# Kernel optimization log

Hardware: AMD Instinct MI355X
Metric: run time of the kernel (lower is better)

Reference implementation:

```python
import jax, jax.numpy as jnp
import numpy as np

FEAT = 1433
HID = 2
NUM_CLASS = 7
EPS = 1e-5  # torch BatchNorm1d default eps


def _bn_softsign(h, gamma, beta):
    # BatchNorm1d in training mode: batch stats over (batch, length) per channel.
    mu = h.mean(axis=(0, 2), keepdims=True)
    var = h.var(axis=(0, 2), keepdims=True)  # biased, matches torch normalization
    hn = (h - mu) * jax.lax.rsqrt(var + EPS)
    hn = hn * gamma[None, :, None] + beta[None, :, None]
    return hn / (1.0 + jnp.abs(hn))  # Softsign


def feature_adjacency(x, y):
    # (x.unsqueeze(-1) * y.unsqueeze(-2)).sum(dim=1) with x channel dim == 1
    # reduces to an outer product of x[:,0] with neighbor.sum over K.
    adj = jnp.einsum('bf,bg->bfg', x.sum(1), y.sum(1))  # [B,F,F]
    adj = adj + jnp.swapaxes(adj, -1, -2)
    adj = jnp.sqrt(adj)
    # row_normalize: divide by sum over dim 1, zero out inf/nan
    norm = adj / adj.sum(axis=1, keepdims=True)
    norm = jnp.where(jnp.isfinite(norm), norm, 0.0)
    return norm + jnp.eye(FEAT, dtype=x.dtype)


def featbrd(x, adj, W, b):
    # adjacency-based feature conv: y[b,c,f] = sum_g adj[(b),f,g] x[b,c,g],
    # then 1x1 conv over channels (Conv1d kernel_size=1).
    if adj.shape[0] == 1:
        y = jnp.einsum('fg,bcg->bcf', adj[0], x)
    else:
        y = jnp.einsum('bfg,bcg->bcf', adj, x)
    return jnp.einsum('oc,bcf->bof', W, y) + b[None, :, None]


def setup_inputs() -> dict:
    key = jax.random.key(0)
    ks = jax.random.split(key, 10)
    B, K = 64, 8
    inp = {
        'x': jax.random.uniform(ks[0], (B, 1, FEAT), dtype=jnp.float32),
        'neighbor': jax.random.uniform(ks[1], (B, K, FEAT), dtype=jnp.float32),
        'adj_buf': jnp.zeros((1, FEAT, FEAT), jnp.float32),
        'W1': jax.random.normal(ks[2], (HID, 1), jnp.float32) * 0.5,
        'b1': jnp.zeros((HID,), jnp.float32),
        'W2': jax.random.normal(ks[3], (HID, HID), jnp.float32) * 0.5,
        'b2': jnp.zeros((HID,), jnp.float32),
        'g1': jnp.ones((HID,), jnp.float32),
        'be1': jnp.zeros((HID,), jnp.float32),
        'g2': jnp.ones((HID,), jnp.float32),
        'be2': jnp.zeros((HID,), jnp.float32),
        'Wc': jax.random.normal(ks[4], (NUM_CLASS, FEAT * HID), jnp.float32) * 0.02,
        'bc': jnp.zeros((NUM_CLASS,), jnp.float32),
    }
    return inp


def reference(x, neighbor, adj_buf, W1, b1, W2, b2, g1, be1, g2, be2, Wc, bc):
    fadj = feature_adjacency(x, neighbor)          # [B,F,F]
    adj_tot = adj_buf + fadj.sum(0)                # [1,F,F] (buffer starts at zero)
    h = _bn_softsign(featbrd(x, fadj, W1, b1), g1, be1)      # [B,HID,F]
    h = _bn_softsign(featbrd(h, adj_tot, W2, b2), g2, be2)   # [B,HID,F]
    flat = h.reshape(h.shape[0], -1)               # Flatten (C then F, row-major)
    return flat @ Wc.T + bc
```

## Files before the change

kernel.cpp:

```cpp
#include <hip/hip_runtime.h>
#include <hip/hip_bf16.h>
#include <math.h>

constexpr int F   = 1433;
constexpr int NB  = 64;
constexpr int KN  = 8;
constexpr int BF  = NB * F;
constexpr float EPS = 1e-5f;

constexpr int SF  = 16;
constexpr int CH  = (F + SF - 1) / SF;
constexpr int SK  = 8;
constexpr int KCH = (F + SK - 1) / SK;
constexpr int FT  = 16;

constexpr int O_YS  = 0;
constexpr int O_Q   = O_YS + BF;
constexpr int O_DP  = O_Q + BF;
constexpr int O_Y1P = O_DP + SF * BF;
constexpr int O_Y1  = O_Y1P + SF * BF;
constexpr int O_HT  = O_Y1 + BF;
constexpr int O_Y2  = O_HT + 128 * F;
constexpr int O_AB  = O_Y2 + 2 * BF;
constexpr int O_ST  = O_AB + 1026752;

__global__ __launch_bounds__(256) void k_D(const float* __restrict__ x,
                                           const float* __restrict__ nbr,
                                           float* __restrict__ DP,
                                           float* __restrict__ ys_out) {
  __shared__ __align__(16) float2 xy[F];
  const int b = blockIdx.x, s = blockIdx.y;
  for (int i = threadIdx.x; i < F; i += 256) {
    const float* p = nbr + (size_t)b * KN * F + i;
    float acc = 0.f;
#pragma unroll
    for (int k = 0; k < KN; ++k) acc += p[k * F];
    xy[i] = make_float2(x[b * F + i], acc);
  }
  __syncthreads();
  if (s == 0) {
    for (int i = threadIdx.x; i < F; i += 256) ys_out[b * F + i] = xy[i].y;
  }
  const int cs = s * CH, cn = min(CH, F - cs);
  float gx[6], gy[6], acc[6] = {};
#pragma unroll
  for (int j = 0; j < 6; ++j) {
    int g = threadIdx.x + 256 * j;
    float2 p = (g < F) ? xy[g] : make_float2(0.f, 0.f);
    gx[j] = p.x; gy[j] = p.y;
  }
  for (int i = 0; i < cn; ++i) {
    float2 p = xy[cs + i];
#pragma unroll
    for (int j = 0; j < 6; ++j)
      acc[j] += __builtin_amdgcn_sqrtf(fmaf(gy[j], p.x, gx[j] * p.y));
  }
#pragma unroll
  for (int j = 0; j < 6; ++j) {
    int g = threadIdx.x + 256 * j;
    if (g < F) DP[(size_t)s * BF + b * F + g] = acc[j];
  }
}

__global__ __launch_bounds__(256) void k_y1(const float* __restrict__ x,
                                            const float* __restrict__ ys,
                                            const float* __restrict__ DP,
                                            float* __restrict__ Y1P,
                                            float* __restrict__ q) {
  __shared__ __align__(16) float4 pl[CH];
  const int b = blockIdx.x, s = blockIdx.y;
  const int cs = s * CH, cn = min(CH, F - cs);
  for (int i = threadIdx.x; i < cn; i += 256) {
    int g = cs + i;
    float d = 0.f;
#pragma unroll
    for (int t = 0; t < SF; ++t) d += DP[(size_t)t * BF + b * F + g];
    float inv = (d > 0.f) ? 1.f / d : 0.f;
    float xv = x[b * F + g], yv = ys[b * F + g];
    pl[i] = make_float4(xv, yv, xv * inv, inv);
    q[b * F + g] = inv;
  }
  __syncthreads();
  float fx[6], fy[6], acc[6] = {};
#pragma unroll
  for (int j = 0; j < 6; ++j) {
    int f = threadIdx.x + 256 * j;
    fx[j] = (f < F) ? x[b * F + f] : 0.f;
    fy[j] = (f < F) ? ys[b * F + f] : 0.f;
  }
  for (int i = 0; i < cn; ++i) {
    float4 p = pl[i];
#pragma unroll
    for (int j = 0; j < 6; ++j)
      acc[j] = fmaf(__builtin_amdgcn_sqrtf(fmaf(fx[j], p.y, fy[j] * p.x)), p.z, acc[j]);
  }
#pragma unroll
  for (int j = 0; j < 6; ++j) {
    int f = threadIdx.x + 256 * j;
    if (f < F) Y1P[(size_t)s * BF + b * F + f] = acc[j];
  }
}

__global__ __launch_bounds__(256) void k_A(const float* __restrict__ x,
                                           const float* __restrict__ ys,
                                           const float* __restrict__ q,
                                           __hip_bfloat16* __restrict__ Ab) {
  __shared__ float2 fxy[FT][NB];
  const int fbase = blockIdx.y * FT;
  for (int i = threadIdx.x; i < FT * NB; i += 256) {
    int b = i >> 4, j = i & 15;
    int f = fbase + j;
    float vx = 0.f, vy = 0.f;
    if (f < F) { vx = x[b * F + f]; vy = ys[b * F + f]; }
    fxy[j][b] = make_float2(vx, vy);
  }
  __syncthreads();
  const int g = blockIdx.x * 256 + threadIdx.x;
  if (g >= F) return;
  float acc[FT] = {};
  for (int b = 0; b < NB; ++b) {
    float gx = x[b * F + g], gy = ys[b * F + g], gq = q[b * F + g];
#pragma unroll
    for (int j = 0; j < FT; ++j) {
      float2 w = fxy[j][b];
      acc[j] = fmaf(__builtin_amdgcn_sqrtf(fmaf(w.x, gy, gx * w.y)), gq, acc[j]);
    }
  }
#pragma unroll
  for (int j = 0; j < FT; ++j) {
    int f = fbase + j;
    if (f < F) Ab[(size_t)f * F + g] = __float2bfloat16(acc[j]);
  }
}

__global__ __launch_bounds__(256) void k_stats1(const float* __restrict__ x,
                                                const float* __restrict__ Y1P,
                                                float* __restrict__ y1,
                                                float* __restrict__ st) {
  float s = 0.f, sq = 0.f;
  for (int i = blockIdx.x * 256 + threadIdx.x; i < BF; i += gridDim.x * 256) {
    float v = x[i];
#pragma unroll
    for (int k = 0; k < SF; ++k) v += Y1P[(size_t)k * BF + i];
    y1[i] = v;
    s += v; sq += v * v;
  }
#pragma unroll
  for (int o = 32; o; o >>= 1) {
    s += __shfl_down(s, o, 64);
    sq += __shfl_down(sq, o, 64);
  }
  __shared__ float ls[4], lq[4];
  int wave = threadIdx.x >> 6, lane = threadIdx.x & 63;
  if (lane == 0) { ls[wave] = s; lq[wave] = sq; }
  __syncthreads();
  if (threadIdx.x == 0) {
    atomicAdd(&st[0], ls[0] + ls[1] + ls[2] + ls[3]);
    atomicAdd(&st[1], lq[0] + lq[1] + lq[2] + lq[3]);
  }
}

__global__ __launch_bounds__(256) void k_h1(const float* __restrict__ y1,
                                            const float* __restrict__ st,
                                            const float* __restrict__ W1,
                                            const float* __restrict__ g1,
                                            const float* __restrict__ be1,
                                            float* __restrict__ Ht,
                                            float* __restrict__ y2) {
  float mu = st[0] / (float)BF;
  float var = st[1] / (float)BF - mu * mu;
  float wa = W1[0], wb = W1[1];
  float k0 = wa * g1[0] / sqrtf(wa * wa * var + EPS);
  float k1 = wb * g1[1] / sqrtf(wb * wb * var + EPS);
  float c0 = -k0 * mu + be1[0];
  float c1 = -k1 * mu + be1[1];

  __shared__ float H[16][132];
  const int f0 = blockIdx.x * 16;
#pragma unroll
  for (int r = 0; r < 4; ++r) {
    int idx = threadIdx.x + r * 256;
    int b = idx >> 4, ff = idx & 15;
    int f = f0 + ff;
    float v = (f < F) ? y1[b * F + f] : 0.f;
    float h0 = fmaf(k0, v, c0); h0 = h0 / (1.f + fabsf(h0));
    float h1 = fmaf(k1, v, c1); h1 = h1 / (1.f + fabsf(h1));
    H[ff][2 * b] = h0;
    H[ff][2 * b + 1] = h1;
  }
  __syncthreads();
#pragma unroll
  for (int r = 0; r < 2; ++r) {
    int idx = threadIdx.x + r * 256;
    int ff = idx >> 5, c4 = (idx & 31) * 4;
    int f = f0 + ff;
    if (f < F) *(float4*)&Ht[f * 128 + c4] = *(const float4*)&H[ff][c4];
  }
#pragma unroll
  for (int r = 0; r < 8; ++r) {
    int idx = threadIdx.x + r * 256;
    int m = idx >> 4, ff = idx & 15;
    int f = f0 + ff;
    if (f < F) y2[m * F + f] = 64.f * H[ff][m];
  }
}

struct Pref { ushort a[4]; float4 h[4]; };

__device__ __forceinline__ void loadRegs(const ushort* __restrict__ Ab,
                                         const float* __restrict__ Ht,
                                         int f0, int ffs, int g4s, int tid,
                                         int gc, Pref& p) {
  int f = min(f0 + ffs, F - 1);
#pragma unroll
  for (int k = 0; k < 4; ++k) {
    int g = min(gc + g4s + k, F - 1);
    p.a[k] = Ab[(size_t)f * F + g];
  }
#pragma unroll
  for (int r = 0; r < 4; ++r) {
    int idx = tid + 256 * r;
    int gi = idx >> 5, c4 = (idx & 31) << 2;
    int g = min(gc + gi, F - 1);
    p.h[r] = *(const float4*)&Ht[g * 128 + c4];
  }
}

__device__ __forceinline__ void storeLDS(float* __restrict__ Al, float* __restrict__ Hl,
                                         int f0, int ffs, int g4s, int tid,
                                         int gc, int ge, const Pref& p) {
  bool fv = (f0 + ffs) < F;
#pragma unroll
  for (int k = 0; k < 4; ++k) {
    int g = gc + g4s + k;
    float v = 0.f;
    if (fv && g < ge) {
      __hip_bfloat16 bb = *(const __hip_bfloat16*)&p.a[k];
      v = __bfloat162float(bb);
    }
    Al[(g4s + k) * 36 + ffs] = v;
  }
#pragma unroll
  for (int r = 0; r < 4; ++r) {
    int idx = tid + 256 * r;
    int gi = idx >> 5, c4 = (idx & 31) << 2;
    float4 h = p.h[r];
    if (gc + gi >= ge) h = make_float4(0.f, 0.f, 0.f, 0.f);
    *(float4*)&Hl[gi * 132 + c4] = h;
  }
}

__global__ __launch_bounds__(256) void k_gemm(const ushort* __restrict__ Ab,
                                              const float* __restrict__ Ht,
                                              float* __restrict__ G2P) {
  __shared__ __align__(16) float Al[2][32 * 36];
  __shared__ __align__(16) float Hl[2][32 * 132];
  const int f0 = blockIdx.x * 32;
  const int gs = blockIdx.y * KCH;
  const int ge = min(gs + KCH, F);
  const int tid = threadIdx.x;
  const int ffs = tid >> 3;
  const int g4s = (tid & 7) * 4;
  const int fsub = (tid & 7) * 4;
  const int msub = (tid >> 3) * 4;
  float acc[4][4] = {};
  const int nch = (ge - gs + 31) >> 5;

  Pref p;
  loadRegs(Ab, Ht, f0, ffs, g4s, tid, gs, p);
  storeLDS(Al[0], Hl[0], f0, ffs, g4s, tid, gs, ge, p);
  __syncthreads();

  for (int c = 0; c < nch; ++c) {
    const int buf = c & 1;
    const bool more = (c + 1 < nch);
    if (more) loadRegs(Ab, Ht, f0, ffs, g4s, tid, gs + (c + 1) * 32, p);
    const float* Ab_ = Al[buf];
    const float* Hb_ = Hl[buf];
#pragma unroll 4
    for (int gi = 0; gi < 32; ++gi) {
      float4 a4 = *(const float4*)&Ab_[gi * 36 + fsub];
      float4 h4 = *(const float4*)&Hb_[gi * 132 + msub];
      float av[4] = {a4.x, a4.y, a4.z, a4.w};
      float hv[4] = {h4.x, h4.y, h4.z, h4.w};
#pragma unroll
      for (int i = 0; i < 4; ++i)
#pragma unroll
        for (int j = 0; j < 4; ++j)
          acc[i][j] = fmaf(av[i], hv[j], acc[i][j]);
    }
    if (more) storeLDS(Al[buf ^ 1], Hl[buf ^ 1], f0, ffs, g4s, tid, gs + (c + 1) * 32, ge, p);
    __syncthreads();
  }

  float* dst = G2P + (size_t)blockIdx.y * 128 * F;
#pragma unroll
  for (int i = 0; i < 4; ++i) {
    int f = f0 + fsub + i;
    if (f < F) {
#pragma unroll
      for (int j = 0; j < 4; ++j)
        dst[(msub + j) * F + f] = acc[i][j];
    }
  }
}

__global__ __launch_bounds__(256) void k_stats2(float* __restrict__ y2,
                                                const float* __restrict__ G2P,
                                                float* __restrict__ st) {
  float su = 0.f, sv = 0.f, suu = 0.f, svv = 0.f, suv = 0.f;
  for (int i = blockIdx.x * 256 + threadIdx.x; i < BF; i += gridDim.x * 256) {
    int b = i / F, f = i - b * F;
    int iu = (2 * b) * F + f, iv = iu + F;
    float u = y2[iu], v = y2[iv];
#pragma unroll
    for (int s = 0; s < SK; ++s) {
      u += G2P[(size_t)s * 128 * F + iu];
      v += G2P[(size_t)s * 128 * F + iv];
    }
    y2[iu] = u; y2[iv] = v;
    su += u; sv += v; suu += u * u; svv += v * v; suv += u * v;
  }
#pragma unroll
  for (int o = 32; o; o >>= 1) {
    su += __shfl_down(su, o, 64);
    sv += __shfl_down(sv, o, 64);
    suu += __shfl_down(suu, o, 64);
    svv += __shfl_down(svv, o, 64);
    suv += __shfl_down(suv, o, 64);
  }
  __shared__ float red[5][4];
  int wave = threadIdx.x >> 6, lane = threadIdx.x & 63;
  if (lane == 0) {
    red[0][wave] = su; red[1][wave] = sv; red[2][wave] = suu;
    red[3][wave] = svv; red[4][wave] = suv;
  }
  __syncthreads();
  if (threadIdx.x == 0) {
    atomicAdd(&st[2], red[0][0] + red[0][1] + red[0][2] + red[0][3]);
    atomicAdd(&st[3], red[1][0] + red[1][1] + red[1][2] + red[1][3]);
    atomicAdd(&st[4], red[2][0] + red[2][1] + red[2][2] + red[2][3]);
    atomicAdd(&st[5], red[3][0] + red[3][1] + red[3][2] + red[3][3]);
    atomicAdd(&st[6], red[4][0] + red[4][1] + red[4][2] + red[4][3]);
  }
}

__global__ __launch_bounds__(256) void k_out(const float* __restrict__ y2,
                                             const float* __restrict__ st,
                                             const float* __restrict__ W2,
                                             const float* __restrict__ b2,
                                             const float* __restrict__ g2,
                                             const float* __restrict__ be2,
                                             const float* __restrict__ Wc,
                                             const float* __restrict__ bc,
                                             float* __restrict__ out) {
  float n = (float)BF;
  float Eu = st[2] / n, Ev = st[3] / n;
  float Euu = st[4] / n, Evv = st[5] / n, Euv = st[6] / n;
  float cA[2], cB[2], cC[2];
#pragma unroll
  for (int o = 0; o < 2; ++o) {
    float w0 = W2[o * 2 + 0], w1 = W2[o * 2 + 1];
    float mean = w0 * Eu + w1 * Ev + b2[o];
    float Eh2 = w0 * w0 * Euu + 2.f * w0 * w1 * Euv + w1 * w1 * Evv +
                2.f * b2[o] * (w0 * Eu + w1 * Ev) + b2[o] * b2[o];
    float var = Eh2 - mean * mean;
    float inv = g2[o] / sqrtf(var + EPS);
    cA[o] = w0 * inv;
    cB[o] = w1 * inv;
    cC[o] = (b2[o] - mean) * inv + be2[o];
  }
  const int b = blockIdx.x;
  float acc[7] = {};
  for (int f = threadIdx.x; f < F; f += 256) {
    float u = y2[(2 * b) * F + f], v = y2[(2 * b + 1) * F + f];
    float h0 = fmaf(cA[0], u, fmaf(cB[0], v, cC[0]));
    h0 = h0 / (1.f + fabsf(h0));
    float h1 = fmaf(cA[1], u, fmaf(cB[1], v, cC[1]));
    h1 = h1 / (1.f + fabsf(h1));
#pragma unroll
    for (int o = 0; o < 7; ++o) acc[o] = fmaf(Wc[o * (2 * F) + f], h0, acc[o]);
#pragma unroll
    for (int o = 0; o < 7; ++o) acc[o] = fmaf(Wc[o * (2 * F) + F + f], h1, acc[o]);
  }
#pragma unroll
  for (int o = 0; o < 7; ++o) {
#pragma unroll
    for (int s = 32; s; s >>= 1) acc[o] += __shfl_down(acc[o], s, 64);
  }
  __shared__ float red[7][4];
  int wave = threadIdx.x >> 6, lane = threadIdx.x & 63;
  if (lane == 0) {
#pragma unroll
    for (int o = 0; o < 7; ++o) red[o][wave] = acc[o];
  }
  __syncthreads();
  if (threadIdx.x < 7) {
    int o = threadIdx.x;
    out[b * 7 + o] = red[o][0] + red[o][1] + red[o][2] + red[o][3] + bc[o];
  }
}

extern "C" void kernel_launch(void* const* d_in, const int* in_sizes, int n_in,
                              void* d_out, int out_size, void* d_ws, size_t ws_size,
                              hipStream_t stream) {
  const float* x    = (const float*)d_in[0];
  const float* nbr  = (const float*)d_in[1];
  const float* W1   = (const float*)d_in[3];
  const float* W2   = (const float*)d_in[5];
  const float* b2   = (const float*)d_in[6];
  const float* g1   = (const float*)d_in[7];
  const float* be1  = (const float*)d_in[8];
  const float* g2   = (const float*)d_in[9];
  const float* be2  = (const float*)d_in[10];
  const float* Wc   = (const float*)d_in[11];
  const float* bc   = (const float*)d_in[12];
  float* out = (float*)d_out;
  float* ws = (float*)d_ws;

  float* ys  = ws + O_YS;
  float* q   = ws + O_Q;
  float* DP  = ws + O_DP;
  float* Y1P = ws + O_Y1P;
  float* y1  = ws + O_Y1;
  float* Ht  = ws + O_HT;
  float* y2  = ws + O_Y2;
  __hip_bfloat16* Ab = (__hip_bfloat16*)(ws + O_AB);
  float* st  = ws + O_ST;

  hipMemsetAsync(st, 0, 64 * sizeof(float), stream);

  k_D     <<<dim3(NB, SF), 256, 0, stream>>>(x, nbr, DP, ys);
  k_y1    <<<dim3(NB, SF), 256, 0, stream>>>(x, ys, DP, Y1P, q);
  k_A     <<<dim3(6, (F + FT - 1) / FT), 256, 0, stream>>>(x, ys, q, Ab);
  k_stats1<<<128, 256, 0, stream>>>(x, Y1P, y1, st);
  k_h1    <<<(F + 15) / 16, 256, 0, stream>>>(y1, st, W1, g1, be1, Ht, y2);
  k_gemm  <<<dim3((F + 31) / 32, SK), 256, 0, stream>>>((const ushort*)Ab, Ht, DP);
  k_stats2<<<128, 256, 0, stream>>>(y2, DP, st);
  k_out   <<<NB, 256, 0, stream>>>(y2, st, W2, b2, g2, be2, Wc, bc, out);
}
```

Before: 213.5 us.

## Fuse adjacency build with stats, fold BN1 into GEMM, pad Ab rows

Merges the A-matrix construction and the first statistics reduction into one heterogeneous launch, and drops the k_h1 kernel: the GEMM now recomputes BN1+softsign from y1 on the fly while loading tiles, and k_stats2 recomputes the residual term. It also packs x, y and inverse norm into a float4 buffer for coalesced reads, pads Ab rows to 1440 for aligned uint2 bf16 loads, and retiles the GEMM K-split to 15 chunks of 96. Double buffering in the GEMM is removed and a few loops get explicit unroll pragmas. These cut launches and intermediate traffic in exchange for redundant elementwise work and less load/compute overlap in the GEMM.

Result: no change. 217.6 us (+1.9%).

```diff
diff --git a/kernel.cpp b/kernel.cpp
--- a/kernel.cpp
+++ b/kernel.cpp
@@ -10,19 +10,22 @@
 
 constexpr int SF  = 16;
 constexpr int CH  = (F + SF - 1) / SF;
-constexpr int SK  = 8;
-constexpr int KCH = (F + SK - 1) / SK;
+constexpr int AbS = 1440;
+constexpr int SK  = 15;
+constexpr int KCH = 96;
 constexpr int FT  = 16;
+constexpr int NAB = 540;
+constexpr int NST = 256;
 
 constexpr int O_YS  = 0;
-constexpr int O_Q   = O_YS + BF;
-constexpr int O_DP  = O_Q + BF;
+constexpr int O_DP  = O_YS + BF;
 constexpr int O_Y1P = O_DP + SF * BF;
-constexpr int O_Y1  = O_Y1P + SF * BF;
-constexpr int O_HT  = O_Y1 + BF;
-constexpr int O_Y2  = O_HT + 128 * F;
-constexpr int O_AB  = O_Y2 + 2 * BF;
-constexpr int O_ST  = O_AB + 1026752;
+constexpr int O_P   = O_Y1P + SF * BF;
+constexpr int O_Y1  = O_P + 4 * BF;
+constexpr int O_Y2  = O_Y1 + BF;
+constexpr int O_G2P = O_Y2 + 2 * BF;
+constexpr int O_AB  = O_G2P + SK * 128 * F;
+constexpr int O_ST  = O_AB + (F * AbS) / 2;
 
 __global__ __launch_bounds__(256) void k_D(const float* __restrict__ x,
                                            const float* __restrict__ nbr,
@@ -49,6 +52,7 @@
     float2 p = (g < F) ? xy[g] : make_float2(0.f, 0.f);
     gx[j] = p.x; gy[j] = p.y;
   }
+#pragma unroll 8
   for (int i = 0; i < cn; ++i) {
     float2 p = xy[cs + i];
 #pragma unroll
@@ -66,7 +70,7 @@
                                             const float* __restrict__ ys,
                                             const float* __restrict__ DP,
                                             float* __restrict__ Y1P,
-                                            float* __restrict__ q) {
+                                            float4* __restrict__ P) {
   __shared__ __align__(16) float4 pl[CH];
   const int b = blockIdx.x, s = blockIdx.y;
   const int cs = s * CH, cn = min(CH, F - cs);
@@ -77,8 +81,9 @@
     for (int t = 0; t < SF; ++t) d += DP[(size_t)t * BF + b * F + g];
     float inv = (d > 0.f) ? 1.f / d : 0.f;
     float xv = x[b * F + g], yv = ys[b * F + g];
-    pl[i] = make_float4(xv, yv, xv * inv, inv);
-    q[b * F + g] = inv;
+    float4 pv = make_float4(xv, yv, xv * inv, inv);
+    pl[i] = pv;
+    P[b * F + g] = pv;
   }
   __syncthreads();
   float fx[6], fy[6], acc[6] = {};
@@ -88,6 +93,7 @@
     fx[j] = (f < F) ? x[b * F + f] : 0.f;
     fy[j] = (f < F) ? ys[b * F + f] : 0.f;
   }
+#pragma unroll 8
   for (int i = 0; i < cn; ++i) {
     float4 p = pl[i];
 #pragma unroll
@@ -101,186 +107,130 @@
   }
 }
 
-__global__ __launch_bounds__(256) void k_A(const float* __restrict__ x,
-                                           const float* __restrict__ ys,
-                                           const float* __restrict__ q,
-                                           __hip_bfloat16* __restrict__ Ab) {
-  __shared__ float2 fxy[FT][NB];
-  const int fbase = blockIdx.y * FT;
-  for (int i = threadIdx.x; i < FT * NB; i += 256) {
-    int b = i >> 4, j = i & 15;
-    int f = fbase + j;
-    float vx = 0.f, vy = 0.f;
-    if (f < F) { vx = x[b * F + f]; vy = ys[b * F + f]; }
-    fxy[j][b] = make_float2(vx, vy);
-  }
-  __syncthreads();
-  const int g = blockIdx.x * 256 + threadIdx.x;
-  if (g >= F) return;
-  float acc[FT] = {};
-  for (int b = 0; b < NB; ++b) {
-    float gx = x[b * F + g], gy = ys[b * F + g], gq = q[b * F + g];
-#pragma unroll
-    for (int j = 0; j < FT; ++j) {
-      float2 w = fxy[j][b];
-      acc[j] = fmaf(__builtin_amdgcn_sqrtf(fmaf(w.x, gy, gx * w.y)), gq, acc[j]);
-    }
-  }
-#pragma unroll
-  for (int j = 0; j < FT; ++j) {
-    int f = fbase + j;
-    if (f < F) Ab[(size_t)f * F + g] = __float2bfloat16(acc[j]);
-  }
-}
-
-__global__ __launch_bounds__(256) void k_stats1(const float* __restrict__ x,
+__global__ __launch_bounds__(256) void k_Astats(const float* __restrict__ x,
+                                                const float* __restrict__ ys,
+                                                const float4* __restrict__ P,
                                                 const float* __restrict__ Y1P,
+                                                __hip_bfloat16* __restrict__ Ab,
                                                 float* __restrict__ y1,
                                                 float* __restrict__ st) {
-  float s = 0.f, sq = 0.f;
-  for (int i = blockIdx.x * 256 + threadIdx.x; i < BF; i += gridDim.x * 256) {
-    float v = x[i];
-#pragma unroll
-    for (int k = 0; k < SF; ++k) v += Y1P[(size_t)k * BF + i];
-    y1[i] = v;
-    s += v; sq += v * v;
-  }
-#pragma unroll
-  for (int o = 32; o; o >>= 1) {
-    s += __shfl_down(s, o, 64);
-    sq += __shfl_down(sq, o, 64);
-  }
-  __shared__ float ls[4], lq[4];
-  int wave = threadIdx.x >> 6, lane = threadIdx.x & 63;
-  if (lane == 0) { ls[wave] = s; lq[wave] = sq; }
-  __syncthreads();
-  if (threadIdx.x == 0) {
-    atomicAdd(&st[0], ls[0] + ls[1] + ls[2] + ls[3]);
-    atomicAdd(&st[1], lq[0] + lq[1] + lq[2] + lq[3]);
-  }
-}
-
-__global__ __launch_bounds__(256) void k_h1(const float* __restrict__ y1,
-                                            const float* __restrict__ st,
-                                            const float* __restrict__ W1,
-                                            const float* __restrict__ g1,
-                                            const float* __restrict__ be1,
-                                            float* __restrict__ Ht,
-                                            float* __restrict__ y2) {
-  float mu = st[0] / (float)BF;
-  float var = st[1] / (float)BF - mu * mu;
-  float wa = W1[0], wb = W1[1];
-  float k0 = wa * g1[0] / sqrtf(wa * wa * var + EPS);
-  float k1 = wb * g1[1] / sqrtf(wb * wb * var + EPS);
-  float c0 = -k0 * mu + be1[0];
-  float c1 = -k1 * mu + be1[1];
-
-  __shared__ float H[16][132];
-  const int f0 = blockIdx.x * 16;
-#pragma unroll
-  for (int r = 0; r < 4; ++r) {
-    int idx = threadIdx.x + r * 256;
-    int b = idx >> 4, ff = idx & 15;
-    int f = f0 + ff;
-    float v = (f < F) ? y1[b * F + f] : 0.f;
-    float h0 = fmaf(k0, v, c0); h0 = h0 / (1.f + fabsf(h0));
-    float h1 = fmaf(k1, v, c1); h1 = h1 / (1.f + fabsf(h1));
-    H[ff][2 * b] = h0;
-    H[ff][2 * b + 1] = h1;
-  }
-  __syncthreads();
-#pragma unroll
-  for (int r = 0; r < 2; ++r) {
-    int idx = threadIdx.x + r * 256;
-    int ff = idx >> 5, c4 = (idx & 31) * 4;
-    int f = f0 + ff;
-    if (f < F) *(float4*)&Ht[f * 128 + c4] = *(const float4*)&H[ff][c4];
-  }
-#pragma unroll
-  for (int r = 0; r < 8; ++r) {
-    int idx = threadIdx.x + r * 256;
-    int m = idx >> 4, ff = idx & 15;
-    int f = f0 + ff;
-    if (f < F) y2[m * F + f] = 64.f * H[ff][m];
-  }
-}
-
-struct Pref { ushort a[4]; float4 h[4]; };
-
-__device__ __forceinline__ void loadRegs(const ushort* __restrict__ Ab,
-                                         const float* __restrict__ Ht,
-                                         int f0, int ffs, int g4s, int tid,
-                                         int gc, Pref& p) {
-  int f = min(f0 + ffs, F - 1);
-#pragma unroll
-  for (int k = 0; k < 4; ++k) {
-    int g = min(gc + g4s + k, F - 1);
-    p.a[k] = Ab[(size_t)f * F + g];
-  }
-#pragma unroll
-  for (int r = 0; r < 4; ++r) {
-    int idx = tid + 256 * r;
-    int gi = idx >> 5, c4 = (idx & 31) << 2;
-    int g = min(gc + gi, F - 1);
-    p.h[r] = *(const float4*)&Ht[g * 128 + c4];
-  }
-}
-
-__device__ __forceinline__ void storeLDS(float* __restrict__ Al, float* __restrict__ Hl,
-                                         int f0, int ffs, int g4s, int tid,
-                                         int gc, int ge, const Pref& p) {
-  bool fv = (f0 + ffs) < F;
-#pragma unroll
-  for (int k = 0; k < 4; ++k) {
-    int g = gc + g4s + k;
-    float v = 0.f;
-    if (fv && g < ge) {
-      __hip_bfloat16 bb = *(const __hip_bfloat16*)&p.a[k];
-      v = __bfloat162float(bb);
-    }
-    Al[(g4s + k) * 36 + ffs] = v;
-  }
-#pragma unroll
-  for (int r = 0; r < 4; ++r) {
-    int idx = tid + 256 * r;
-    int gi = idx >> 5, c4 = (idx & 31) << 2;
-    float4 h = p.h[r];
-    if (gc + gi >= ge) h = make_float4(0.f, 0.f, 0.f, 0.f);
-    *(float4*)&Hl[gi * 132 + c4] = h;
+  const int bid = blockIdx.x;
+  if (bid < NAB) {
+    __shared__ float2 fxy[FT][NB];
+    const int gx = bid % 6, fy = bid / 6;
+    const int fbase = fy * FT;
+    for (int i = threadIdx.x; i < FT * NB; i += 256) {
+      int b = i >> 4, j = i & 15;
+      int f = fbase + j;
+      float vx = 0.f, vy = 0.f;
+      if (f < F) { vx = x[b * F + f]; vy = ys[b * F + f]; }
+      fxy[j][b] = make_float2(vx, vy);
+    }
+    __syncthreads();
+    const int g = gx * 256 + threadIdx.x;
+    if (g >= AbS) return;
+    if (g < F) {
+      float acc[FT] = {};
+#pragma unroll 2
+      for (int b = 0; b < NB; ++b) {
+        float4 p = P[b * F + g];
+#pragma unroll
+        for (int j = 0; j < FT; ++j) {
+          float2 w = fxy[j][b];
+          acc[j] = fmaf(__builtin_amdgcn_sqrtf(fmaf(w.x, p.y, p.x * w.y)), p.w, acc[j]);
+        }
+      }
+#pragma unroll
+      for (int j = 0; j < FT; ++j) {
+        int f = fbase + j;
+        if (f < F) Ab[(size_t)f * AbS + g] = __float2bfloat16(acc[j]);
+      }
+    } else {
+#pragma unroll
+      for (int j = 0; j < FT; ++j) {
+        int f = fbase + j;
+        if (f < F) Ab[(size_t)f * AbS + g] = __float2bfloat16(0.f);
+      }
+    }
+  } else {
+    const int sid = bid - NAB;
+    float s = 0.f, sq = 0.f;
+    for (int i = sid * 256 + threadIdx.x; i < BF; i += NST * 256) {
+      float v = x[i];
+#pragma unroll
+      for (int k = 0; k < SF; ++k) v += Y1P[(size_t)k * BF + i];
+      y1[i] = v;
+      s += v; sq += v * v;
+    }
+#pragma unroll
+    for (int o = 32; o; o >>= 1) {
+      s += __shfl_down(s, o, 64);
+      sq += __shfl_down(sq, o, 64);
+    }
+    __shared__ float ls[4], lq[4];
+    int wave = threadIdx.x >> 6, lane = threadIdx.x & 63;
+    if (lane == 0) { ls[wave] = s; lq[wave] = sq; }
+    __syncthreads();
+    if (threadIdx.x == 0) {
+      atomicAdd(&st[0], ls[0] + ls[1] + ls[2] + ls[3]);
+      atomicAdd(&st[1], lq[0] + lq[1] + lq[2] + lq[3]);
+    }
   }
 }
 
 __global__ __launch_bounds__(256) void k_gemm(const ushort* __restrict__ Ab,
-                                              const float* __restrict__ Ht,
+                                              const float* __restrict__ y1,
+                                              const float* __restrict__ st,
+                                              const float* __restrict__ W1,
+                                              const float* __restrict__ g1,
+                                              const float* __restrict__ be1,
                                               float* __restrict__ G2P) {
-  __shared__ __align__(16) float Al[2][32 * 36];
-  __shared__ __align__(16) float Hl[2][32 * 132];
+  const float mu = st[0] / (float)BF;
+  const float var = st[1] / (float)BF - mu * mu;
+  const float wa = W1[0], wb = W1[1];
+  const float k0 = wa * g1[0] / sqrtf(wa * wa * var + EPS);
+  const float k1 = wb * g1[1] / sqrtf(wb * wb * var + EPS);
+  const float c0 = -k0 * mu + be1[0];
+  const float c1 = -k1 * mu + be1[1];
+
+  __shared__ __align__(16) float Al[32 * 36];
+  __shared__ __align__(16) float Hl[32 * 132];
   const int f0 = blockIdx.x * 32;
   const int gs = blockIdx.y * KCH;
-  const int ge = min(gs + KCH, F);
   const int tid = threadIdx.x;
   const int ffs = tid >> 3;
   const int g4s = (tid & 7) * 4;
+  const int hb = tid & 7;
+  const int hg = tid >> 3;
   const int fsub = (tid & 7) * 4;
   const int msub = (tid >> 3) * 4;
   float acc[4][4] = {};
-  const int nch = (ge - gs + 31) >> 5;
-
-  Pref p;
-  loadRegs(Ab, Ht, f0, ffs, g4s, tid, gs, p);
-  storeLDS(Al[0], Hl[0], f0, ffs, g4s, tid, gs, ge, p);
-  __syncthreads();
-
-  for (int c = 0; c < nch; ++c) {
-    const int buf = c & 1;
-    const bool more = (c + 1 < nch);
-    if (more) loadRegs(Ab, Ht, f0, ffs, g4s, tid, gs + (c + 1) * 32, p);
-    const float* Ab_ = Al[buf];
-    const float* Hb_ = Hl[buf];
+
+  for (int c = 0; c < 3; ++c) {
+    const int gb = gs + c * 32;
+    {
+      const int f = f0 + ffs;
+      uint2 av = make_uint2(0u, 0u);
+      if (f < F) av = *(const uint2*)&Ab[(size_t)f * AbS + gb + g4s];
+      Al[(g4s + 0) * 36 + ffs] = __uint_as_float(av.x << 16);
+      Al[(g4s + 1) * 36 + ffs] = __uint_as_float(av.x & 0xffff0000u);
+      Al[(g4s + 2) * 36 + ffs] = __uint_as_float(av.y << 16);
+      Al[(g4s + 3) * 36 + ffs] = __uint_as_float(av.y & 0xffff0000u);
+    }
+#pragma unroll
+    for (int r = 0; r < 8; ++r) {
+      const int b = hb + 8 * r;
+      const int gl = min(gb + hg, F - 1);
+      const float v = y1[b * F + gl];
+      float h0 = fmaf(k0, v, c0); h0 = h0 / (1.f + fabsf(h0));
+      float h1 = fmaf(k1, v, c1); h1 = h1 / (1.f + fabsf(h1));
+      *(float2*)&Hl[hg * 132 + 2 * b] = make_float2(h0, h1);
+    }
+    __syncthreads();
 #pragma unroll 4
     for (int gi = 0; gi < 32; ++gi) {
-      float4 a4 = *(const float4*)&Ab_[gi * 36 + fsub];
-      float4 h4 = *(const float4*)&Hb_[gi * 132 + msub];
+      float4 a4 = *(const float4*)&Al[gi * 36 + fsub];
+      float4 h4 = *(const float4*)&Hl[gi * 132 + msub];
       float av[4] = {a4.x, a4.y, a4.z, a4.w};
       float hv[4] = {h4.x, h4.y, h4.z, h4.w};
 #pragma unroll
@@ -289,7 +239,6 @@
         for (int j = 0; j < 4; ++j)
           acc[i][j] = fmaf(av[i], hv[j], acc[i][j]);
     }
-    if (more) storeLDS(Al[buf ^ 1], Hl[buf ^ 1], f0, ffs, g4s, tid, gs + (c + 1) * 32, ge, p);
     __syncthreads();
   }
 
@@ -305,14 +254,30 @@
   }
 }
 
-__global__ __launch_bounds__(256) void k_stats2(float* __restrict__ y2,
+__global__ __launch_bounds__(256) void k_stats2(const float* __restrict__ y1,
                                                 const float* __restrict__ G2P,
-                                                float* __restrict__ st) {
+                                                const float* __restrict__ st,
+                                                const float* __restrict__ W1,
+                                                const float* __restrict__ g1,
+                                                const float* __restrict__ be1,
+                                                float* __restrict__ y2,
+                                                float* __restrict__ stw) {
+  const float mu = st[0] / (float)BF;
+  const float var = st[1] / (float)BF - mu * mu;
+  const float wa = W1[0], wb = W1[1];
+  const float k0 = wa * g1[0] / sqrtf(wa * wa * var + EPS);
+  const float k1 = wb * g1[1] / sqrtf(wb * wb * var + EPS);
+  const float c0 = -k0 * mu + be1[0];
+  const float c1 = -k1 * mu + be1[1];
+
   float su = 0.f, sv = 0.f, suu = 0.f, svv = 0.f, suv = 0.f;
   for (int i = blockIdx.x * 256 + threadIdx.x; i < BF; i += gridDim.x * 256) {
     int b = i / F, f = i - b * F;
+    float w = y1[i];
+    float h0 = fmaf(k0, w, c0); h0 = h0 / (1.f + fabsf(h0));
+    float h1 = fmaf(k1, w, c1); h1 = h1 / (1.f + fabsf(h1));
     int iu = (2 * b) * F + f, iv = iu + F;
-    float u = y2[iu], v = y2[iv];
+    float u = 64.f * h0, v = 64.f * h1;
 #pragma unroll
     for (int s = 0; s < SK; ++s) {
       u += G2P[(size_t)s * 128 * F + iu];
@@ -337,11 +302,11 @@
   }
   __syncthreads();
   if (threadIdx.x == 0) {
-    atomicAdd(&st[2], red[0][0] + red[0][1] + red[0][2] + red[0][3]);
-    atomicAdd(&st[3], red[1][0] + red[1][1] + red[1][2] + red[1][3]);
-    atomicAdd(&st[4], red[2][0] + red[2][1] + red[2][2] + red[2][3]);
-    atomicAdd(&st[5], red[3][0] + red[3][1] + red[3][2] + red[3][3]);
-    atomicAdd(&st[6], red[4][0] + red[4][1] + red[4][2] + red[4][3]);
+    atomicAdd(&stw[2], red[0][0] + red[0][1] + red[0][2] + red[0][3]);
+    atomicAdd(&stw[3], red[1][0] + red[1][1] + red[1][2] + red[1][3]);
+    atomicAdd(&stw[4], red[2][0] + red[2][1] + red[2][2] + red[2][3]);
+    atomicAdd(&stw[5], red[3][0] + red[3][1] + red[3][2] + red[3][3]);
+    atomicAdd(&stw[6], red[4][0] + red[4][1] + red[4][2] + red[4][3]);
   }
 }
 
@@ -418,24 +383,22 @@
   float* out = (float*)d_out;
   float* ws = (float*)d_ws;
 
-  float* ys  = ws + O_YS;
-  float* q   = ws + O_Q;
-  float* DP  = ws + O_DP;
-  float* Y1P = ws + O_Y1P;
-  float* y1  = ws + O_Y1;
-  float* Ht  = ws + O_HT;
-  float* y2  = ws + O_Y2;
+  float*  ys  = ws + O_YS;
+  float*  DP  = ws + O_DP;
+  float*  Y1P = ws + O_Y1P;
+  float4* P   = (float4*)(ws + O_P);
+  float*  y1  = ws + O_Y1;
+  float*  y2  = ws + O_Y2;
+  float*  G2P = ws + O_G2P;
   __hip_bfloat16* Ab = (__hip_bfloat16*)(ws + O_AB);
-  float* st  = ws + O_ST;
+  float*  st  = ws + O_ST;
 
   hipMemsetAsync(st, 0, 64 * sizeof(float), stream);
 
   k_D     <<<dim3(NB, SF), 256, 0, stream>>>(x, nbr, DP, ys);
-  k_y1    <<<dim3(NB, SF), 256, 0, stream>>>(x, ys, DP, Y1P, q);
-  k_A     <<<dim3(6, (F + FT - 1) / FT), 256, 0, stream>>>(x, ys, q, Ab);
-  k_stats1<<<128, 256, 0, stream>>>(x, Y1P, y1, st);
-  k_h1    <<<(F + 15) / 16, 256, 0, stream>>>(y1, st, W1, g1, be1, Ht, y2);
-  k_gemm  <<<dim3((F + 31) / 32, SK), 256, 0, stream>>>((const ushort*)Ab, Ht, DP);
-  k_stats2<<<128, 256, 0, stream>>>(y2, DP, st);
+  k_y1    <<<dim3(NB, SF), 256, 0, stream>>>(x, ys, DP, Y1P, P);
+  k_Astats<<<NAB + NST, 256, 0, stream>>>(x, ys, P, Y1P, Ab, y1, st);
+  k_gemm  <<<dim3(45, SK), 256, 0, stream>>>((const ushort*)Ab, y1, st, W1, g1, be1, G2P);
+  k_stats2<<<NST, 256, 0, stream>>>(y1, G2P, st, W1, g1, be1, y2, st);
   k_out   <<<NB, 256, 0, stream>>>(y2, st, W2, b2, g2, be2, Wc, bc, out);
 }
```
